# Performance work log

Hardware: AMD Instinct MI355X
Metric: run time of the kernel (lower is better)

## Reference

```python
import jax, jax.numpy as jnp
import numpy as np

B, K, C, L = 16, 8, 64, 2048
OFFSET = 2.0  # self.offset in Coupling
EPS = 1e-7    # clamp for logit stability (flows' safe_log analogue)


def setup_inputs() -> dict:
    key = jax.random.key(0)
    ks = jax.random.split(key, 6)
    return {
        "x_change": jax.random.normal(ks[0], (B, C, L), jnp.float32),
        "a": jax.random.normal(ks[1], (B, C, L), jnp.float32),
        "b": jax.random.normal(ks[2], (B, C, L), jnp.float32),
        "pi": jax.random.normal(ks[3], (B, K, C, L), jnp.float32),
        "mu": jax.random.normal(ks[4], (B, K, C, L), jnp.float32),
        "s": jax.random.normal(ks[5], (B, K, C, L), jnp.float32) * 0.1,  # log-scales
        "sldj": jnp.zeros((B,), jnp.float32),
    }


def reference(x_change, a, b, pi, mu, s, sldj):
    # scale = sigmoid(a + offset) + (1 - sigmoid(offset))
    sig_off = 1.0 - jax.nn.sigmoid(jnp.float32(OFFSET))
    scale = jax.nn.sigmoid(a + OFFSET) + sig_off                      # [B,C,L]

    logpi = jax.nn.log_softmax(pi, axis=1)                            # [B,K,C,L]
    z = (x_change[:, None] - mu) * jnp.exp(-s)                        # [B,K,C,L]

    # logistic.mixture_log_cdf: logsumexp_k(log pi_k + log sigmoid(z_k))
    log_cdf = jax.scipy.special.logsumexp(logpi + jax.nn.log_sigmoid(z), axis=1)
    u = jnp.clip(jnp.exp(log_cdf), EPS, 1.0 - EPS)                    # [B,C,L]

    # logistic.inverse (forward): logit, with ldj = -log(u) - log(1-u)
    y = jnp.log(u) - jnp.log1p(-u)
    scale_ldj = -jnp.log(u) - jnp.log1p(-u)

    # logistic.mixture_log_pdf: logsumexp_k(log pi_k + z - s - 2 softplus(z))
    log_pdf = jax.scipy.special.logsumexp(
        logpi + z - s - 2.0 * jax.nn.softplus(z), axis=1)             # [B,C,L]

    sldj_out = sldj + jnp.sum(
        (log_pdf + scale_ldj + jnp.log(scale)).reshape(sldj.shape[0], -1), axis=-1)
    out = (y + b) * scale                                             # [B,C,L]
    return out, sldj_out
```

## Files before the change

kernel.cpp:

```cpp
#include <hip/hip_runtime.h>

#define BB 16
#define KK 8
#define CC 64
#define LL 2048

constexpr int CL = CC * LL;
constexpr int QUADS_PER_BATCH = CL / 4;
constexpr int NBLOCKS = (BB * QUADS_PER_BATCH) / 256;

#define SIG_OFF 0.11920292202211755f
#define EPS_U 1e-7f

__device__ __forceinline__ float softplus_f(float x) {
    return fmaxf(x, 0.f) + log1pf(__expf(-fabsf(x)));
}

__device__ __forceinline__ float get4(const float4& v, int e) {
    switch (e) {
        case 0: return v.x;
        case 1: return v.y;
        case 2: return v.z;
        default: return v.w;
    }
}

__device__ __forceinline__ void set4(float4& v, int e, float f) {
    switch (e) {
        case 0: v.x = f; break;
        case 1: v.y = f; break;
        case 2: v.z = f; break;
        default: v.w = f; break;
    }
}

__global__ void init_sldj_kernel(const float* __restrict__ sldj_in,
                                 float* __restrict__ sldj_out) {
    int i = threadIdx.x;
    if (i < BB) sldj_out[i] = sldj_in[i];
}

__global__ __launch_bounds__(256) void coupling_kernel(
    const float* __restrict__ x,
    const float* __restrict__ a,
    const float* __restrict__ bv,
    const float* __restrict__ pi,
    const float* __restrict__ mu,
    const float* __restrict__ s,
    float* __restrict__ out,
    float* __restrict__ sldj_out) {

    const int idx = blockIdx.x * 256 + threadIdx.x;
    const int b   = idx >> 15;
    const int rem = idx & (QUADS_PER_BATCH - 1);
    const int base = b * CL + rem * 4;

    const float4 x4 = *(const float4*)(x + base);
    const float4 a4 = *(const float4*)(a + base);
    const float4 b4 = *(const float4*)(bv + base);

    float4 pi4[KK], mu4[KK], s4[KK];
#pragma unroll
    for (int k = 0; k < KK; ++k) {
        const int kb = (b * KK + k) * CL + rem * 4;
        pi4[k] = *(const float4*)(pi + kb);
        mu4[k] = *(const float4*)(mu + kb);
        s4[k]  = *(const float4*)(s  + kb);
    }

    float contrib = 0.f;
    float4 out4;

#pragma unroll
    for (int e = 0; e < 4; ++e) {
        const float xe = get4(x4, e);
        const float ae = get4(a4, e);
        const float be = get4(b4, e);

        float piv[KK], argc[KK], argp[KK];
#pragma unroll
        for (int k = 0; k < KK; ++k) {
            const float p  = get4(pi4[k], e);
            const float sk = get4(s4[k], e);
            const float z  = (xe - get4(mu4[k], e)) * __expf(-sk);
            const float sp = softplus_f(z);
            piv[k]  = p;
            argc[k] = p + (z - sp);
            argp[k] = p + z - sk - 2.f * sp;
        }

        float m_pi = piv[0], m_c = argc[0], m_p = argp[0];
#pragma unroll
        for (int k = 1; k < KK; ++k) {
            m_pi = fmaxf(m_pi, piv[k]);
            m_c  = fmaxf(m_c,  argc[k]);
            m_p  = fmaxf(m_p,  argp[k]);
        }
        float s_pi = 0.f, s_c = 0.f, s_p = 0.f;
#pragma unroll
        for (int k = 0; k < KK; ++k) {
            s_pi += __expf(piv[k]  - m_pi);
            s_c  += __expf(argc[k] - m_c);
            s_p  += __expf(argp[k] - m_p);
        }
        const float lse_pi  = m_pi + __logf(s_pi);
        const float log_cdf = (m_c + __logf(s_c)) - lse_pi;
        const float log_pdf = (m_p + __logf(s_p)) - lse_pi;

        float u = __expf(log_cdf);
        u = fminf(fmaxf(u, EPS_U), 1.f - EPS_U);
        const float lu   = __logf(u);
        const float l1mu = log1pf(-u);
        const float y        = lu - l1mu;
        const float ldj_term = -lu - l1mu;

        const float sc = 1.f / (1.f + __expf(-(ae + 2.f))) + SIG_OFF;

        set4(out4, e, (y + be) * sc);
        contrib += log_pdf + ldj_term + __logf(sc);
    }

    *(float4*)(out + base) = out4;

#pragma unroll
    for (int off = 32; off > 0; off >>= 1)
        contrib += __shfl_down(contrib, off, 64);

    __shared__ float wsum[4];
    const int lane = threadIdx.x & 63;
    const int wid  = threadIdx.x >> 6;
    if (lane == 0) wsum[wid] = contrib;
    __syncthreads();
    if (threadIdx.x == 0) {
        const float t = wsum[0] + wsum[1] + wsum[2] + wsum[3];
        atomicAdd(&sldj_out[b], t);
    }
}

extern "C" void kernel_launch(void* const* d_in, const int* in_sizes, int n_in,
                              void* d_out, int out_size, void* d_ws, size_t ws_size,
                              hipStream_t stream) {
    const float* x    = (const float*)d_in[0];
    const float* a    = (const float*)d_in[1];
    const float* bv   = (const float*)d_in[2];
    const float* pi   = (const float*)d_in[3];
    const float* mu   = (const float*)d_in[4];
    const float* s    = (const float*)d_in[5];
    const float* sldj = (const float*)d_in[6];

    float* out      = (float*)d_out;
    float* sldj_out = out + (size_t)BB * CL;

    init_sldj_kernel<<<1, 64, 0, stream>>>(sldj, sldj_out);
    coupling_kernel<<<NBLOCKS, 256, 0, stream>>>(x, a, bv, pi, mu, s, out, sldj_out);
}
```

Baseline: 234.2 us.

## Replace per-component logsumexp with linear-domain mixture sums and streamed loads

```diff
diff --git a/kernel.cpp b/kernel.cpp
--- a/kernel.cpp
+++ b/kernel.cpp
@@ -10,11 +10,9 @@
 constexpr int NBLOCKS = (BB * QUADS_PER_BATCH) / 256;
 
 #define SIG_OFF 0.11920292202211755f
-#define EPS_U 1e-7f
+#define LOG_EPS -16.11809565095832f
 
-__device__ __forceinline__ float softplus_f(float x) {
-    return fmaxf(x, 0.f) + log1pf(__expf(-fabsf(x)));
-}
+__device__ __forceinline__ float frcp(float x) { return __builtin_amdgcn_rcpf(x); }
 
 __device__ __forceinline__ float get4(const float4& v, int e) {
     switch (e) {
@@ -59,13 +57,38 @@
     const float4 a4 = *(const float4*)(a + base);
     const float4 b4 = *(const float4*)(bv + base);
 
-    float4 pi4[KK], mu4[KK], s4[KK];
+    float Spi[4] = {0.f, 0.f, 0.f, 0.f};
+    float Nc[4]  = {0.f, 0.f, 0.f, 0.f};
+    float N1[4]  = {0.f, 0.f, 0.f, 0.f};
+    float Np[4]  = {0.f, 0.f, 0.f, 0.f};
+
 #pragma unroll
     for (int k = 0; k < KK; ++k) {
         const int kb = (b * KK + k) * CL + rem * 4;
-        pi4[k] = *(const float4*)(pi + kb);
-        mu4[k] = *(const float4*)(mu + kb);
-        s4[k]  = *(const float4*)(s  + kb);
+        const float4 pi4 = *(const float4*)(pi + kb);
+        const float4 mu4 = *(const float4*)(mu + kb);
+        const float4 s4  = *(const float4*)(s  + kb);
+
+#pragma unroll
+        for (int e = 0; e < 4; ++e) {
+            const float p      = get4(pi4, e);
+            const float m      = get4(mu4, e);
+            const float sk     = get4(s4, e);
+            const float invstd = __expf(-sk);
+            const float z      = (get4(x4, e) - m) * invstd;
+
+            const float t  = __expf(-fabsf(z));
+            const float r  = frcp(1.f + t);
+            const float tr = t * r;
+            const float sig  = (z >= 0.f) ? r  : tr;
+            const float osig = (z >= 0.f) ? tr : r;
+
+            const float ek = __expf(p);
+            Spi[e] += ek;
+            Nc[e]  += ek * sig;
+            N1[e]  += ek * osig;
+            Np[e]  += ek * invstd * sig * osig;
+        }
     }
 
     float contrib = 0.f;
@@ -73,50 +96,19 @@
 
 #pragma unroll
     for (int e = 0; e < 4; ++e) {
-        const float xe = get4(x4, e);
-        const float ae = get4(a4, e);
-        const float be = get4(b4, e);
+        const float lSpi = __logf(Spi[e]);
+        const float lu   = fmaxf(__logf(Nc[e]) - lSpi, LOG_EPS);
+        const float lomu = fmaxf(__logf(N1[e]) - lSpi, LOG_EPS);
+        const float y        = lu - lomu;
+        const float ldj_term = -lu - lomu;
+        const float log_pdf  = __logf(Np[e]) - lSpi;
 
-        float piv[KK], argc[KK], argp[KK];
-#pragma unroll
-        for (int k = 0; k < KK; ++k) {
-            const float p  = get4(pi4[k], e);
-            const float sk = get4(s4[k], e);
-            const float z  = (xe - get4(mu4[k], e)) * __expf(-sk);
-            const float sp = softplus_f(z);
-            piv[k]  = p;
-            argc[k] = p + (z - sp);
-            argp[k] = p + z - sk - 2.f * sp;
-        }
+        const float ae = get4(a4, e) + 2.f;
+        const float t2 = __expf(-fabsf(ae));
+        const float r2 = frcp(1.f + t2);
+        const float sc = ((ae >= 0.f) ? r2 : t2 * r2) + SIG_OFF;
 
-        float m_pi = piv[0], m_c = argc[0], m_p = argp[0];
-#pragma unroll
-        for (int k = 1; k < KK; ++k) {
-            m_pi = fmaxf(m_pi, piv[k]);
-            m_c  = fmaxf(m_c,  argc[k]);
-            m_p  = fmaxf(m_p,  argp[k]);
-        }
-        float s_pi = 0.f, s_c = 0.f, s_p = 0.f;
-#pragma unroll
-        for (int k = 0; k < KK; ++k) {
-            s_pi += __expf(piv[k]  - m_pi);
-            s_c  += __expf(argc[k] - m_c);
-            s_p  += __expf(argp[k] - m_p);
-        }
-        const float lse_pi  = m_pi + __logf(s_pi);
-        const float log_cdf = (m_c + __logf(s_c)) - lse_pi;
-        const float log_pdf = (m_p + __logf(s_p)) - lse_pi;
-
-        float u = __expf(log_cdf);
-        u = fminf(fmaxf(u, EPS_U), 1.f - EPS_U);
-        const float lu   = __logf(u);
-        const float l1mu = log1pf(-u);
-        const float y        = lu - l1mu;
-        const float ldj_term = -lu - l1mu;
-
-        const float sc = 1.f / (1.f + __expf(-(ae + 2.f))) + SIG_OFF;
-
-        set4(out4, e, (y + be) * sc);
+        set4(out4, e, (y + get4(b4, e)) * sc);
         contrib += log_pdf + ldj_term + __logf(sc);
     }
 
@@ -132,8 +124,7 @@
     if (lane == 0) wsum[wid] = contrib;
     __syncthreads();
     if (threadIdx.x == 0) {
-        const float t = wsum[0] + wsum[1] + wsum[2] + wsum[3];
-        atomicAdd(&sldj_out[b], t);
+        atomicAdd(&sldj_out[b], wsum[0] + wsum[1] + wsum[2] + wsum[3]);
     }
 }
 
```

Measured after the change: 231.9 us. About the same (-1.0%).
